# Optimization experiments

Measured on AMD Instinct MI355X. Metric: run time of the kernel, lower is better.

## Reference

```python
import jax, jax.numpy as jnp
import numpy as np

B, H, W, C = 2, 128, 128, 128
NS = 8                      # attn_num_splits
WH, WW = H // NS, W // NS   # window size 16x16
SH, SW = WH // 2, WW // 2   # shift sizes
HID = 2 * C * 4             # ffn hidden (in_channels = 2*d_model, expansion 4)
EPS = 1e-5


def _make_swin_mask():
    # Standard shifted-window attention mask: -100 between different regions.
    img = np.zeros((H, W), np.int32)
    cnt = 0
    for hs in (slice(0, -WH), slice(-WH, -SH), slice(-SH, None)):
        for ws in (slice(0, -WW), slice(-WW, -SW), slice(-SW, None)):
            img[hs, ws] = cnt
            cnt += 1
    ids = img.reshape(NS, WH, NS, WW).transpose(0, 2, 1, 3).reshape(NS * NS, WH * WW)
    mask = np.where(ids[:, None, :] != ids[:, :, None], -100.0, 0.0).astype(np.float32)
    return jnp.asarray(mask)  # (64, 256, 256)


def _layernorm(x, g, b):
    m = jnp.mean(x, axis=-1, keepdims=True)
    v = jnp.mean(jnp.square(x - m), axis=-1, keepdims=True)
    return (x - m) * jax.lax.rsqrt(v + EPS) * g + b


def setup_inputs() -> dict:
    key = jax.random.key(0)
    ks = jax.random.split(key, 8)
    s = 1.0 / np.sqrt(C)
    return {
        "source": jax.random.normal(ks[0], (B, H * W, C), jnp.float32),
        "target": jax.random.normal(ks[1], (B, H * W, C), jnp.float32),
        "Wq": jax.random.normal(ks[2], (C, C), jnp.float32) * s,
        "Wk": jax.random.normal(ks[3], (C, C), jnp.float32) * s,
        "Wv": jax.random.normal(ks[4], (C, C), jnp.float32) * s,
        "Wm": jax.random.normal(ks[5], (C, C), jnp.float32) * s,
        "g1": jnp.ones((C,), jnp.float32),
        "b1": jnp.zeros((C,), jnp.float32),
        "W1": jax.random.normal(ks[6], (2 * C, HID), jnp.float32) * (1.0 / np.sqrt(2 * C)),
        "W2": jax.random.normal(ks[7], (HID, C), jnp.float32) * (1.0 / np.sqrt(HID)),
        "g2": jnp.ones((C,), jnp.float32),
        "b2": jnp.zeros((C,), jnp.float32),
        "shifted_window_attn_mask": _make_swin_mask(),
        "height": H,
        "width": W,
        "attn_num_splits": NS,
    }


def reference(source, target, Wq, Wk, Wv, Wm, g1, b1, W1, W2, g2, b2,
              shifted_window_attn_mask, height, width, attn_num_splits):
    b, L, c = source.shape
    h, w, ns = height, width, attn_num_splits
    wh, ww = h // ns, w // ns
    sh, sw = wh // 2, ww // 2

    q = source @ Wq
    k = target @ Wk
    v = target @ Wv

    def to_windows(x):
        # (b, h*w, c) -> shifted -> (b, nWin, wh*ww, c)
        x = x.reshape(b, h, w, c)
        x = jnp.roll(x, (-sh, -sw), axis=(1, 2))
        x = x.reshape(b, ns, wh, ns, ww, c).transpose(0, 1, 3, 2, 4, 5)
        return x.reshape(b, ns * ns, wh * ww, c)

    qw, kw, vw = to_windows(q), to_windows(k), to_windows(v)
    scores = jnp.einsum('bnlc,bnmc->bnlm', qw, kw) / (c ** 0.5)
    scores = scores + shifted_window_attn_mask[None]  # broadcast over batch
    attn = jax.nn.softmax(scores, axis=-1)
    out = jnp.einsum('bnlm,bnmc->bnlc', attn, vw)

    # merge windows back and undo the shift
    out = out.reshape(b, ns, ns, wh, ww, c).transpose(0, 1, 3, 2, 4, 5).reshape(b, h, w, c)
    out = jnp.roll(out, (sh, sw), axis=(1, 2)).reshape(b, h * w, c)

    message = _layernorm(out @ Wm, g1, b1)
    ffn_in = jnp.concatenate([source, message], axis=-1)
    message = jax.nn.gelu(ffn_in @ W1, approximate=False) @ W2
    message = _layernorm(message, g2, b2)
    return source + message
```

## Files before the change

kernel.cpp:

```cpp
#include <hip/hip_runtime.h>
#include <math.h>
#include <stdint.h>


typedef unsigned short u16;
typedef __attribute__((ext_vector_type(8))) short bf16x8;
typedef __attribute__((ext_vector_type(4))) float f32x4;
typedef __attribute__((ext_vector_type(4))) short u16x4;

__device__ __forceinline__ u16 f2b(float f) {
    unsigned int i = __float_as_uint(f);
    unsigned int r = (i + 0x7fffu + ((i >> 16) & 1u)) >> 16;
    return (u16)r;
}

__device__ __forceinline__ float fast_gelu(float x) {
    float y = fabsf(x) * 0.70710678118f;
    float t = __builtin_amdgcn_rcpf(fmaf(0.3275911f, y, 1.0f));
    float p = fmaf(fmaf(fmaf(fmaf(1.061405429f, t, -1.453152027f), t,
                             1.421413741f), t, -0.284496736f), t, 0.254829592f) * t;
    float e = __expf(-y * y);
    float erf_abs = fmaf(-p, e, 1.0f);
    float s = copysignf(erf_abs, x);
    return 0.5f * x * (1.0f + s);
}

__device__ __forceinline__ void cp16(const void* g, void* l) {
    auto* gp = reinterpret_cast<const __attribute__((address_space(1))) unsigned int*>(
        reinterpret_cast<uintptr_t>(g));
    auto* lp = reinterpret_cast<__attribute__((address_space(3))) unsigned int*>(
        reinterpret_cast<uintptr_t>(l));
    __builtin_amdgcn_global_load_lds(gp, lp, 16, 0, 0);
}

__device__ __forceinline__ int win_map(int gm) {
    int b = gm >> 14, rr = gm & 16383;
    int win = rr >> 8, t = rr & 255;
    int wi = win >> 3, wj = win & 7, i = t >> 4, j = t & 15;
    int h = (wi * 16 + i + 8) & 127;
    int w = (wj * 16 + j + 8) & 127;
    return (b << 14) + h * 128 + w;
}

__global__ __launch_bounds__(256, 2)
void gemm_qkv(const u16* __restrict__ srcb, const u16* __restrict__ tgtb,
              const u16* __restrict__ Bt, u16* __restrict__ qw,
              u16* __restrict__ kw, u16* __restrict__ vwt)
{
    __shared__ __align__(16) u16 SMEM[32768];
    u16* As = SMEM;
    u16* Bs = SMEM + 16384;
    u16* Ts = SMEM;

    const int tid = threadIdx.x;
    const int w = tid >> 6, lane = tid & 63;
    const int lm = lane & 15, q = lane >> 4;
    const int wm = w >> 1, wn = w & 1;
    const int m0 = blockIdx.x * 128;
    const int y = blockIdx.y;
    const u16* Ab = (y == 0) ? srcb : tgtb;

#pragma unroll
    for (int s = 0; s < 4; ++s)
#pragma unroll
        for (int i = 0; i < 2; ++i) {
            int row = w * 32 + i * 16 + (lane >> 2);
            int kc = s * 32 + (lane & 3) * 8;
            cp16(Ab + (size_t)win_map(m0 + row) * 128 + kc,
                 (void*)(As + (s * 128 + w * 32 + i * 16) * 32));
            cp16(Bt + (size_t)(y * 128 + row) * 128 + kc,
                 (void*)(Bs + (s * 128 + w * 32 + i * 16) * 32));
        }
    __syncthreads();

    f32x4 acc[4][4] = {};
#pragma unroll
    for (int s = 0; s < 4; ++s) {
        bf16x8 af[4], bfr[4];
#pragma unroll
        for (int t = 0; t < 4; ++t)
            af[t] = *(const bf16x8*)(As + (s * 128 + wm * 64 + t * 16 + lm) * 32 + q * 8);
#pragma unroll
        for (int t = 0; t < 4; ++t)
            bfr[t] = *(const bf16x8*)(Bs + (s * 128 + wn * 64 + t * 16 + lm) * 32 + q * 8);
#pragma unroll
        for (int mt = 0; mt < 4; ++mt)
#pragma unroll
            for (int nt = 0; nt < 4; ++nt)
                acc[mt][nt] = __builtin_amdgcn_mfma_f32_16x16x32_bf16(
                    af[mt], bfr[nt], acc[mt][nt], 0, 0, 0);
    }

    __syncthreads();
#pragma unroll
    for (int mt = 0; mt < 4; ++mt)
#pragma unroll
        for (int nt = 0; nt < 4; ++nt)
#pragma unroll
            for (int r = 0; r < 4; ++r) {
                int rowl = wm * 64 + mt * 16 + q * 4 + r;
                int col = wn * 64 + nt * 16 + lm;
                int idx = (y == 2) ? col * 136 + rowl : rowl * 136 + col;
                Ts[idx] = f2b(acc[mt][nt][r]);
            }
    __syncthreads();
    const int c8 = (tid & 15) * 8;
#pragma unroll
    for (int i = 0; i < 8; ++i) {
        int rr = i * 16 + (tid >> 4);
        bf16x8 t = *(const bf16x8*)(Ts + rr * 136 + c8);
        if (y == 2) {
            int wix = m0 >> 8, tok0 = m0 & 255;
            *(bf16x8*)(vwt + (size_t)wix * 32768 + (size_t)rr * 256 + tok0 + c8) = t;
        } else {
            u16* Cv = (y == 0) ? qw : kw;
            *(bf16x8*)(Cv + (size_t)(m0 + rr) * 128 + c8) = t;
        }
    }
}

__global__ __launch_bounds__(256, 2)
void gemm_ffn1(const u16* __restrict__ A0, const u16* __restrict__ A1,
               const u16* __restrict__ Bt, u16* __restrict__ C)
{
    __shared__ __align__(16) u16 SMEM[32768];
    u16* As = SMEM;
    u16* Bs = SMEM + 16384;
    u16* Ts = SMEM;

    const int tid = threadIdx.x;
    const int w = tid >> 6, lane = tid & 63;
    const int lm = lane & 15, q = lane >> 4;
    const int wm = w >> 1, wn = w & 1;
    const int m0 = blockIdx.x * 128, n0 = blockIdx.y * 128;

    f32x4 acc[4][4] = {};
#pragma unroll
    for (int kt2 = 0; kt2 < 2; ++kt2) {
        __syncthreads();
        const u16* Ab = kt2 ? A1 : A0;
#pragma unroll
        for (int s = 0; s < 4; ++s)
#pragma unroll
            for (int i = 0; i < 2; ++i) {
                int row = w * 32 + i * 16 + (lane >> 2);
                int kc = s * 32 + (lane & 3) * 8;
                cp16(Ab + (size_t)(m0 + row) * 128 + kc,
                     (void*)(As + (s * 128 + w * 32 + i * 16) * 32));
                cp16(Bt + (size_t)(n0 + row) * 256 + kt2 * 128 + kc,
                     (void*)(Bs + (s * 128 + w * 32 + i * 16) * 32));
            }
        __syncthreads();
#pragma unroll
        for (int s = 0; s < 4; ++s) {
            bf16x8 af[4], bfr[4];
#pragma unroll
            for (int t = 0; t < 4; ++t)
                af[t] = *(const bf16x8*)(As + (s * 128 + wm * 64 + t * 16 + lm) * 32 + q * 8);
#pragma unroll
            for (int t = 0; t < 4; ++t)
                bfr[t] = *(const bf16x8*)(Bs + (s * 128 + wn * 64 + t * 16 + lm) * 32 + q * 8);
#pragma unroll
            for (int mt = 0; mt < 4; ++mt)
#pragma unroll
                for (int nt = 0; nt < 4; ++nt)
                    acc[mt][nt] = __builtin_amdgcn_mfma_f32_16x16x32_bf16(
                        af[mt], bfr[nt], acc[mt][nt], 0, 0, 0);
        }
    }

    __syncthreads();
#pragma unroll
    for (int mt = 0; mt < 4; ++mt)
#pragma unroll
        for (int nt = 0; nt < 4; ++nt)
#pragma unroll
            for (int r = 0; r < 4; ++r) {
                int rowl = wm * 64 + mt * 16 + q * 4 + r;
                int col = wn * 64 + nt * 16 + lm;
                Ts[rowl * 136 + col] = f2b(fast_gelu(acc[mt][nt][r]));
            }
    __syncthreads();
    const int c8 = (tid & 15) * 8;
#pragma unroll
    for (int i = 0; i < 8; ++i) {
        int rr = i * 16 + (tid >> 4);
        bf16x8 t = *(const bf16x8*)(Ts + rr * 136 + c8);
        *(bf16x8*)(C + (size_t)(m0 + rr) * 1024 + n0 + c8) = t;
    }
}

template <int KSTAGES, bool RESID>
__global__ __launch_bounds__(256, 3)
void gemm_ln(const u16* __restrict__ A, const u16* __restrict__ Bt,
             const float* __restrict__ g, const float* __restrict__ bb,
             const float* __restrict__ resid, void* __restrict__ outv)
{
    __shared__ __align__(16) u16 SMEM[25088];
    u16* As = SMEM;
    u16* Bs = SMEM + 8192;
    float* stats = (float*)(SMEM + 24576);
    u16* Ts = SMEM;

    const int tid = threadIdx.x;
    const int w = tid >> 6, lane = tid & 63;
    const int lm = lane & 15, q = lane >> 4;
    const int wm = w >> 1, wn = w & 1;
    const int m0 = blockIdx.x * 64;
    const int K = KSTAGES * 128;

    f32x4 acc[2][4] = {};
#pragma unroll
    for (int kt2 = 0; kt2 < KSTAGES; ++kt2) {
        __syncthreads();
#pragma unroll
        for (int s = 0; s < 4; ++s) {
            int kc = kt2 * 128 + s * 32 + (lane & 3) * 8;
            int arow = w * 16 + (lane >> 2);
            cp16(A + (size_t)(m0 + arow) * K + kc,
                 (void*)(As + (s * 64 + w * 16) * 32));
#pragma unroll
            for (int i = 0; i < 2; ++i) {
                int brow = w * 32 + i * 16 + (lane >> 2);
                cp16(Bt + (size_t)brow * K + kc,
                     (void*)(Bs + (s * 128 + w * 32 + i * 16) * 32));
            }
        }
        __syncthreads();
#pragma unroll
        for (int s = 0; s < 4; ++s) {
            bf16x8 af[2], bfr[4];
#pragma unroll
            for (int t = 0; t < 2; ++t)
                af[t] = *(const bf16x8*)(As + (s * 64 + wm * 32 + t * 16 + lm) * 32 + q * 8);
#pragma unroll
            for (int t = 0; t < 4; ++t)
                bfr[t] = *(const bf16x8*)(Bs + (s * 128 + wn * 64 + t * 16 + lm) * 32 + q * 8);
#pragma unroll
            for (int mt = 0; mt < 2; ++mt)
#pragma unroll
                for (int nt = 0; nt < 4; ++nt)
                    acc[mt][nt] = __builtin_amdgcn_mfma_f32_16x16x32_bf16(
                        af[mt], bfr[nt], acc[mt][nt], 0, 0, 0);
        }
    }

#pragma unroll
    for (int mt = 0; mt < 2; ++mt)
#pragma unroll
        for (int r = 0; r < 4; ++r) {
            float s1 = 0.f, s2 = 0.f;
#pragma unroll
            for (int nt = 0; nt < 4; ++nt) {
                float v = acc[mt][nt][r];
                s1 += v; s2 += v * v;
            }
            s1 += __shfl_xor(s1, 1); s2 += __shfl_xor(s2, 1);
            s1 += __shfl_xor(s1, 2); s2 += __shfl_xor(s2, 2);
            s1 += __shfl_xor(s1, 4); s2 += __shfl_xor(s2, 4);
            s1 += __shfl_xor(s1, 8); s2 += __shfl_xor(s2, 8);
            if (lm == 0) {
                int row = wm * 32 + mt * 16 + q * 4 + r;
                stats[row * 4 + wn * 2] = s1;
                stats[row * 4 + wn * 2 + 1] = s2;
            }
        }
    __syncthreads();

    float gv[4], bv[4];
#pragma unroll
    for (int nt = 0; nt < 4; ++nt) {
        int col = wn * 64 + nt * 16 + lm;
        gv[nt] = g[col]; bv[nt] = bb[col];
    }

#pragma unroll
    for (int mt = 0; mt < 2; ++mt)
#pragma unroll
        for (int r = 0; r < 4; ++r) {
            int row = wm * 32 + mt * 16 + q * 4 + r;
            f32x4 st = *(const f32x4*)(stats + row * 4);
            float mean = (st[0] + st[2]) * (1.f / 128.f);
            float var = fmaxf((st[1] + st[3]) * (1.f / 128.f) - mean * mean, 0.f);
            float rs = rsqrtf(var + 1e-5f);
#pragma unroll
            for (int nt = 0; nt < 4; ++nt) {
                int col = wn * 64 + nt * 16 + lm;
                float yv = (acc[mt][nt][r] - mean) * rs * gv[nt] + bv[nt];
                if (RESID) {
                    size_t gi = (size_t)(m0 + row) * 128 + col;
                    ((float*)outv)[gi] = yv + resid[gi];
                } else {
                    Ts[row * 136 + col] = f2b(yv);
                }
            }
        }
    if (!RESID) {
        __syncthreads();
        const int c8 = (tid & 15) * 8;
#pragma unroll
        for (int i = 0; i < 4; ++i) {
            int rr = i * 16 + (tid >> 4);
            bf16x8 t = *(const bf16x8*)(Ts + rr * 136 + c8);
            *(bf16x8*)((u16*)outv + (size_t)(m0 + rr) * 128 + c8) = t;
        }
    }
}

__global__ __launch_bounds__(256)
void attn_k(const u16* __restrict__ qw, const u16* __restrict__ kw,
            const u16* __restrict__ vt, u16* __restrict__ om)
{
    __shared__ __align__(16) u16 Ps[64 * 264];

    const int tid = threadIdx.x, w = tid >> 6, lane = tid & 63;
    const int lm = lane & 15, q = lane >> 4;
    const int bid = blockIdx.x;
    const int qc = bid & 3, win = (bid >> 2) & 63, b = bid >> 8;
    const int wi = win >> 3, wj = win & 7;
    const int q0 = qc * 64;
    const size_t wbase = (size_t)(b * 64 + win);
    const u16* kwb = kw + wbase * 256 * 128;
    const u16* qwb = qw + wbase * 256 * 128;
    const u16* vtb = vt + wbase * 128 * 256;

    bf16x8 af[4];
    const u16* qrow = qwb + (size_t)(q0 + w * 16 + lm) * 128;
#pragma unroll
    for (int kt = 0; kt < 4; ++kt)
        af[kt] = *(const bf16x8*)(qrow + kt * 32 + q * 8);

    f32x4 s[16];
#pragma unroll
    for (int nt = 0; nt < 16; ++nt) { f32x4 z = {0.f, 0.f, 0.f, 0.f}; s[nt] = z; }
#pragma unroll
    for (int kt = 0; kt < 4; ++kt)
#pragma unroll
        for (int nt = 0; nt < 16; ++nt) {
            bf16x8 bf = *(const bf16x8*)(kwb + (size_t)(nt * 16 + lm) * 128 + kt * 32 + q * 8);
            s[nt] = __builtin_amdgcn_mfma_f32_16x16x32_bf16(af[kt], bf, s[nt], 0, 0, 0);
        }

    int idk[16];
#pragma unroll
    for (int nt = 0; nt < 16; ++nt) {
        int rh = (wi == 7) ? ((nt >= 8) ? 2 : 1) : 0;
        int rw = (wj == 7) ? ((lm >= 8) ? 2 : 1) : 0;
        idk[nt] = rh * 3 + rw;
    }
    const float scale = 0.08838834764831845f;
#pragma unroll
    for (int r = 0; r < 4; ++r) {
        int tq = q0 + w * 16 + q * 4 + r;
        int iq = tq >> 4, jq = tq & 15;
        int rhq = (wi == 7) ? ((iq >= 8) ? 2 : 1) : 0;
        int rwq = (wj == 7) ? ((jq >= 8) ? 2 : 1) : 0;
        int idq = rhq * 3 + rwq;
        float sv[16];
        float mx = -1e30f;
#pragma unroll
        for (int nt = 0; nt < 16; ++nt) {
            float x = s[nt][r] * scale + ((idq != idk[nt]) ? -100.f : 0.f);
            sv[nt] = x; mx = fmaxf(mx, x);
        }
        mx = fmaxf(mx, __shfl_xor(mx, 1));
        mx = fmaxf(mx, __shfl_xor(mx, 2));
        mx = fmaxf(mx, __shfl_xor(mx, 4));
        mx = fmaxf(mx, __shfl_xor(mx, 8));
        float sum = 0.f;
#pragma unroll
        for (int nt = 0; nt < 16; ++nt) { float e = __expf(sv[nt] - mx); sv[nt] = e; sum += e; }
        sum += __shfl_xor(sum, 1);
        sum += __shfl_xor(sum, 2);
        sum += __shfl_xor(sum, 4);
        sum += __shfl_xor(sum, 8);
        float inv = 1.0f / sum;
#pragma unroll
        for (int nt = 0; nt < 16; ++nt)
            Ps[(w * 16 + q * 4 + r) * 264 + nt * 16 + lm] = f2b(sv[nt] * inv);
    }
    __syncthreads();

    f32x4 o[8];
#pragma unroll
    for (int nt = 0; nt < 8; ++nt) { f32x4 z = {0.f, 0.f, 0.f, 0.f}; o[nt] = z; }
#pragma unroll
    for (int tt = 0; tt < 8; ++tt) {
        bf16x8 pf = *(const bf16x8*)(Ps + (w * 16 + lm) * 264 + tt * 32 + q * 8);
#pragma unroll
        for (int nt = 0; nt < 8; ++nt) {
            bf16x8 vf = *(const bf16x8*)(vtb + (size_t)(nt * 16 + lm) * 256 + tt * 32 + q * 8);
            o[nt] = __builtin_amdgcn_mfma_f32_16x16x32_bf16(pf, vf, o[nt], 0, 0, 0);
        }
    }

    __syncthreads();
    u16* Ts = Ps;
#pragma unroll
    for (int r = 0; r < 4; ++r) {
        int rl = w * 16 + q * 4 + r;
#pragma unroll
        for (int nt = 0; nt < 8; ++nt)
            Ts[rl * 136 + nt * 16 + lm] = f2b(o[nt][r]);
    }
    __syncthreads();
    const int c8 = (tid & 15) * 8;
#pragma unroll
    for (int i = 0; i < 4; ++i) {
        int rr = i * 16 + (tid >> 4);
        int t = q0 + rr;
        int ii = t >> 4, jj = t & 15;
        int h = (wi * 16 + ii + 8) & 127;
        int w2 = (wj * 16 + jj + 8) & 127;
        bf16x8 v = *(const bf16x8*)(Ts + rr * 136 + c8);
        *(bf16x8*)(om + ((size_t)b * 16384 + h * 128 + w2) * 128 + c8) = v;
    }
}

__global__ void prep_all(const float* __restrict__ Wq, const float* __restrict__ Wk,
                         const float* __restrict__ Wv, const float* __restrict__ Wm,
                         const float* __restrict__ W1, const float* __restrict__ W2,
                         const float* __restrict__ src, const float* __restrict__ tgt,
                         u16* __restrict__ ws, u16* __restrict__ srcb,
                         u16* __restrict__ tgtb)
{
    int bx = blockIdx.x;
    if (bx < 1792) {
        int idx = bx * 256 + threadIdx.x;
        if (idx < 65536) {
            int m = idx >> 14, e = idx & 16383;
            const float* sp = (m == 0) ? Wq : (m == 1) ? Wk : (m == 2) ? Wv : Wm;
            int k = e >> 7, n = e & 127;
            ws[m * 16384 + n * 128 + k] = f2b(sp[e]);
        } else if (idx < 65536 + 262144) {
            int e = idx - 65536;
            int k = e >> 10, n = e & 1023;
            ws[65536 + n * 256 + k] = f2b(W1[e]);
        } else {
            int e = idx - (65536 + 262144);
            int k = e >> 7, n = e & 127;
            ws[327680 + n * 1024 + k] = f2b(W2[e]);
        }
    } else {
        int idx = (bx - 1792) * 256 + threadIdx.x;
        const float* s; u16* d; int i;
        if (idx < 1048576) { s = src; d = srcb; i = idx * 4; }
        else               { s = tgt; d = tgtb; i = (idx - 1048576) * 4; }
        f32x4 v = *(const f32x4*)(s + i);
        u16x4 o; o[0] = f2b(v[0]); o[1] = f2b(v[1]); o[2] = f2b(v[2]); o[3] = f2b(v[3]);
        *(u16x4*)(d + i) = o;
    }
}

#define OFF_WQT  0u
#define OFF_WMT  49152u
#define OFF_W1T  65536u
#define OFF_W2T  327680u
#define OFF_SRCB 458752u
#define OFF_TGTB 4653056u
#define OFF_QW   8847360u
#define OFF_KW   13041664u
#define OFF_VWT  17235968u
#define OFF_ATTN 21430272u
#define OFF_HID  25624576u
#define OFF_MSGB 8847360u

extern "C" void kernel_launch(void* const* d_in, const int* in_sizes, int n_in,
                              void* d_out, int out_size, void* d_ws, size_t ws_size,
                              hipStream_t stream)
{
    (void)in_sizes; (void)n_in; (void)out_size; (void)ws_size;
    const float* source = (const float*)d_in[0];
    const float* target = (const float*)d_in[1];
    const float* Wq = (const float*)d_in[2];
    const float* Wk = (const float*)d_in[3];
    const float* Wv = (const float*)d_in[4];
    const float* Wm = (const float*)d_in[5];
    const float* g1 = (const float*)d_in[6];
    const float* b1 = (const float*)d_in[7];
    const float* W1 = (const float*)d_in[8];
    const float* W2 = (const float*)d_in[9];
    const float* g2 = (const float*)d_in[10];
    const float* b2 = (const float*)d_in[11];
    u16* ws = (u16*)d_ws;
    float* out = (float*)d_out;

    prep_all<<<9984, 256, 0, stream>>>(Wq, Wk, Wv, Wm, W1, W2, source, target,
                                       ws, ws + OFF_SRCB, ws + OFF_TGTB);
    gemm_qkv<<<dim3(256, 3), 256, 0, stream>>>(
        ws + OFF_SRCB, ws + OFF_TGTB, ws + OFF_WQT,
        ws + OFF_QW, ws + OFF_KW, ws + OFF_VWT);
    attn_k<<<512, 256, 0, stream>>>(ws + OFF_QW, ws + OFF_KW, ws + OFF_VWT, ws + OFF_ATTN);
    gemm_ln<1, false><<<512, 256, 0, stream>>>(
        ws + OFF_ATTN, ws + OFF_WMT, g1, b1, nullptr, (void*)(ws + OFF_MSGB));
    gemm_ffn1<<<dim3(256, 8), 256, 0, stream>>>(
        ws + OFF_SRCB, ws + OFF_MSGB, ws + OFF_W1T, ws + OFF_HID);
    gemm_ln<8, true><<<512, 256, 0, stream>>>(
        ws + OFF_HID, ws + OFF_W2T, g2, b2, source, (void*)out);
}
```

Before: 232.8 us.

## Fuse Wm projection and LayerNorm into attention, switch FFN1 to 32x32 MFMA

The message projection and first LayerNorm move into the attention kernel epilogue, so the separate gemm_ln launch and the round trip of the attention output through global memory go away. FFN1 now uses 32x32x16 MFMA tiles, replaces the erf-based GELU with a cheaper rational approximation, and writes scalar bf16 directly instead of staging through LDS. The prep kernel now iterates in output order, so transposed weight writes become contiguous while the reads become strided. Risks are lower GELU accuracy, uncoalesced 2-byte global stores in the FFN1 and attention epilogues, and the attention kernel reading Wm fragments straight from global memory.

```diff
diff --git a/kernel.cpp b/kernel.cpp
--- a/kernel.cpp
+++ b/kernel.cpp
@@ -6,6 +6,7 @@
 typedef unsigned short u16;
 typedef __attribute__((ext_vector_type(8))) short bf16x8;
 typedef __attribute__((ext_vector_type(4))) float f32x4;
+typedef __attribute__((ext_vector_type(16))) float f32x16;
 typedef __attribute__((ext_vector_type(4))) short u16x4;
 
 __device__ __forceinline__ u16 f2b(float f) {
@@ -14,15 +15,13 @@
     return (u16)r;
 }
 
-__device__ __forceinline__ float fast_gelu(float x) {
+__device__ __forceinline__ float gelu_e(float x) {
     float y = fabsf(x) * 0.70710678118f;
-    float t = __builtin_amdgcn_rcpf(fmaf(0.3275911f, y, 1.0f));
-    float p = fmaf(fmaf(fmaf(fmaf(1.061405429f, t, -1.453152027f), t,
-                             1.421413741f), t, -0.284496736f), t, 0.254829592f) * t;
-    float e = __expf(-y * y);
-    float erf_abs = fmaf(-p, e, 1.0f);
-    float s = copysignf(erf_abs, x);
-    return 0.5f * x * (1.0f + s);
+    float u = fmaf(y, fmaf(y, fmaf(y, fmaf(y, 0.078108f, 0.000972f),
+                                   0.230389f), 0.278393f), 1.0f);
+    u = u * u; u = u * u;
+    float r = __builtin_amdgcn_rcpf(u);
+    return fmaxf(x, 0.f) - 0.5f * fabsf(x) * r;
 }
 
 __device__ __forceinline__ void cp16(const void* g, void* l) {
@@ -126,15 +125,14 @@
     __shared__ __align__(16) u16 SMEM[32768];
     u16* As = SMEM;
     u16* Bs = SMEM + 16384;
-    u16* Ts = SMEM;
 
     const int tid = threadIdx.x;
     const int w = tid >> 6, lane = tid & 63;
-    const int lm = lane & 15, q = lane >> 4;
+    const int l32 = lane & 31, lh = lane >> 5;
     const int wm = w >> 1, wn = w & 1;
     const int m0 = blockIdx.x * 128, n0 = blockIdx.y * 128;
 
-    f32x4 acc[4][4] = {};
+    f32x16 acc[2][2] = {};
 #pragma unroll
     for (int kt2 = 0; kt2 < 2; ++kt2) {
         __syncthreads();
@@ -152,164 +150,46 @@
             }
         __syncthreads();
 #pragma unroll
-        for (int s = 0; s < 4; ++s) {
-            bf16x8 af[4], bfr[4];
-#pragma unroll
-            for (int t = 0; t < 4; ++t)
-                af[t] = *(const bf16x8*)(As + (s * 128 + wm * 64 + t * 16 + lm) * 32 + q * 8);
-#pragma unroll
-            for (int t = 0; t < 4; ++t)
-                bfr[t] = *(const bf16x8*)(Bs + (s * 128 + wn * 64 + t * 16 + lm) * 32 + q * 8);
-#pragma unroll
-            for (int mt = 0; mt < 4; ++mt)
-#pragma unroll
-                for (int nt = 0; nt < 4; ++nt)
-                    acc[mt][nt] = __builtin_amdgcn_mfma_f32_16x16x32_bf16(
-                        af[mt], bfr[nt], acc[mt][nt], 0, 0, 0);
-        }
-    }
-
-    __syncthreads();
-#pragma unroll
-    for (int mt = 0; mt < 4; ++mt)
-#pragma unroll
-        for (int nt = 0; nt < 4; ++nt)
-#pragma unroll
-            for (int r = 0; r < 4; ++r) {
-                int rowl = wm * 64 + mt * 16 + q * 4 + r;
-                int col = wn * 64 + nt * 16 + lm;
-                Ts[rowl * 136 + col] = f2b(fast_gelu(acc[mt][nt][r]));
-            }
-    __syncthreads();
-    const int c8 = (tid & 15) * 8;
-#pragma unroll
-    for (int i = 0; i < 8; ++i) {
-        int rr = i * 16 + (tid >> 4);
-        bf16x8 t = *(const bf16x8*)(Ts + rr * 136 + c8);
-        *(bf16x8*)(C + (size_t)(m0 + rr) * 1024 + n0 + c8) = t;
-    }
-}
-
-template <int KSTAGES, bool RESID>
-__global__ __launch_bounds__(256, 3)
-void gemm_ln(const u16* __restrict__ A, const u16* __restrict__ Bt,
-             const float* __restrict__ g, const float* __restrict__ bb,
-             const float* __restrict__ resid, void* __restrict__ outv)
-{
-    __shared__ __align__(16) u16 SMEM[25088];
-    u16* As = SMEM;
-    u16* Bs = SMEM + 8192;
-    float* stats = (float*)(SMEM + 24576);
-    u16* Ts = SMEM;
-
-    const int tid = threadIdx.x;
-    const int w = tid >> 6, lane = tid & 63;
-    const int lm = lane & 15, q = lane >> 4;
-    const int wm = w >> 1, wn = w & 1;
-    const int m0 = blockIdx.x * 64;
-    const int K = KSTAGES * 128;
-
-    f32x4 acc[2][4] = {};
-#pragma unroll
-    for (int kt2 = 0; kt2 < KSTAGES; ++kt2) {
-        __syncthreads();
-#pragma unroll
-        for (int s = 0; s < 4; ++s) {
-            int kc = kt2 * 128 + s * 32 + (lane & 3) * 8;
-            int arow = w * 16 + (lane >> 2);
-            cp16(A + (size_t)(m0 + arow) * K + kc,
-                 (void*)(As + (s * 64 + w * 16) * 32));
-#pragma unroll
-            for (int i = 0; i < 2; ++i) {
-                int brow = w * 32 + i * 16 + (lane >> 2);
-                cp16(Bt + (size_t)brow * K + kc,
-                     (void*)(Bs + (s * 128 + w * 32 + i * 16) * 32));
-            }
-        }
-        __syncthreads();
-#pragma unroll
-        for (int s = 0; s < 4; ++s) {
-            bf16x8 af[2], bfr[4];
-#pragma unroll
-            for (int t = 0; t < 2; ++t)
-                af[t] = *(const bf16x8*)(As + (s * 64 + wm * 32 + t * 16 + lm) * 32 + q * 8);
-#pragma unroll
-            for (int t = 0; t < 4; ++t)
-                bfr[t] = *(const bf16x8*)(Bs + (s * 128 + wn * 64 + t * 16 + lm) * 32 + q * 8);
-#pragma unroll
-            for (int mt = 0; mt < 2; ++mt)
-#pragma unroll
-                for (int nt = 0; nt < 4; ++nt)
-                    acc[mt][nt] = __builtin_amdgcn_mfma_f32_16x16x32_bf16(
-                        af[mt], bfr[nt], acc[mt][nt], 0, 0, 0);
-        }
+        for (int s = 0; s < 4; ++s)
+#pragma unroll
+            for (int kc = 0; kc < 2; ++kc) {
+                bf16x8 af[2], bfr[2];
+#pragma unroll
+                for (int mt = 0; mt < 2; ++mt)
+                    af[mt] = *(const bf16x8*)(As + (s * 128 + wm * 64 + mt * 32 + l32) * 32
+                                              + kc * 16 + lh * 8);
+#pragma unroll
+                for (int nt = 0; nt < 2; ++nt)
+                    bfr[nt] = *(const bf16x8*)(Bs + (s * 128 + wn * 64 + nt * 32 + l32) * 32
+                                               + kc * 16 + lh * 8);
+#pragma unroll
+                for (int mt = 0; mt < 2; ++mt)
+#pragma unroll
+                    for (int nt = 0; nt < 2; ++nt)
+                        acc[mt][nt] = __builtin_amdgcn_mfma_f32_32x32x16_bf16(
+                            af[mt], bfr[nt], acc[mt][nt], 0, 0, 0);
+            }
     }
 
 #pragma unroll
     for (int mt = 0; mt < 2; ++mt)
 #pragma unroll
-        for (int r = 0; r < 4; ++r) {
-            float s1 = 0.f, s2 = 0.f;
-#pragma unroll
-            for (int nt = 0; nt < 4; ++nt) {
-                float v = acc[mt][nt][r];
-                s1 += v; s2 += v * v;
-            }
-            s1 += __shfl_xor(s1, 1); s2 += __shfl_xor(s2, 1);
-            s1 += __shfl_xor(s1, 2); s2 += __shfl_xor(s2, 2);
-            s1 += __shfl_xor(s1, 4); s2 += __shfl_xor(s2, 4);
-            s1 += __shfl_xor(s1, 8); s2 += __shfl_xor(s2, 8);
-            if (lm == 0) {
-                int row = wm * 32 + mt * 16 + q * 4 + r;
-                stats[row * 4 + wn * 2] = s1;
-                stats[row * 4 + wn * 2 + 1] = s2;
-            }
-        }
-    __syncthreads();
-
-    float gv[4], bv[4];
-#pragma unroll
-    for (int nt = 0; nt < 4; ++nt) {
-        int col = wn * 64 + nt * 16 + lm;
-        gv[nt] = g[col]; bv[nt] = bb[col];
-    }
-
-#pragma unroll
-    for (int mt = 0; mt < 2; ++mt)
-#pragma unroll
-        for (int r = 0; r < 4; ++r) {
-            int row = wm * 32 + mt * 16 + q * 4 + r;
-            f32x4 st = *(const f32x4*)(stats + row * 4);
-            float mean = (st[0] + st[2]) * (1.f / 128.f);
-            float var = fmaxf((st[1] + st[3]) * (1.f / 128.f) - mean * mean, 0.f);
-            float rs = rsqrtf(var + 1e-5f);
-#pragma unroll
-            for (int nt = 0; nt < 4; ++nt) {
-                int col = wn * 64 + nt * 16 + lm;
-                float yv = (acc[mt][nt][r] - mean) * rs * gv[nt] + bv[nt];
-                if (RESID) {
-                    size_t gi = (size_t)(m0 + row) * 128 + col;
-                    ((float*)outv)[gi] = yv + resid[gi];
-                } else {
-                    Ts[row * 136 + col] = f2b(yv);
-                }
-            }
-        }
-    if (!RESID) {
-        __syncthreads();
-        const int c8 = (tid & 15) * 8;
-#pragma unroll
-        for (int i = 0; i < 4; ++i) {
-            int rr = i * 16 + (tid >> 4);
-            bf16x8 t = *(const bf16x8*)(Ts + rr * 136 + c8);
-            *(bf16x8*)((u16*)outv + (size_t)(m0 + rr) * 128 + c8) = t;
-        }
-    }
+        for (int nt = 0; nt < 2; ++nt) {
+            int col = n0 + wn * 64 + nt * 32 + l32;
+            int rbase = m0 + wm * 64 + mt * 32 + 4 * lh;
+#pragma unroll
+            for (int r = 0; r < 16; ++r) {
+                int row = rbase + (r & 3) + 8 * (r >> 2);
+                C[(size_t)row * 1024 + col] = f2b(gelu_e(acc[mt][nt][r]));
+            }
+        }
 }
 
 __global__ __launch_bounds__(256)
-void attn_k(const u16* __restrict__ qw, const u16* __restrict__ kw,
-            const u16* __restrict__ vt, u16* __restrict__ om)
+void attn_msg(const u16* __restrict__ qw, const u16* __restrict__ kw,
+              const u16* __restrict__ vt, const u16* __restrict__ wmt,
+              const float* __restrict__ g, const float* __restrict__ bb,
+              u16* __restrict__ msgb)
 {
     __shared__ __align__(16) u16 Ps[64 * 264];
 
@@ -395,26 +275,158 @@
     }
 
     __syncthreads();
-    u16* Ts = Ps;
+    u16* Ot = Ps;
 #pragma unroll
     for (int r = 0; r < 4; ++r) {
         int rl = w * 16 + q * 4 + r;
 #pragma unroll
         for (int nt = 0; nt < 8; ++nt)
-            Ts[rl * 136 + nt * 16 + lm] = f2b(o[nt][r]);
-    }
-    __syncthreads();
-    const int c8 = (tid & 15) * 8;
-#pragma unroll
-    for (int i = 0; i < 4; ++i) {
-        int rr = i * 16 + (tid >> 4);
-        int t = q0 + rr;
+            Ot[rl * 136 + nt * 16 + lm] = f2b(o[nt][r]);
+    }
+    __syncthreads();
+
+    f32x4 macc[8];
+#pragma unroll
+    for (int n2 = 0; n2 < 8; ++n2) { f32x4 z = {0.f, 0.f, 0.f, 0.f}; macc[n2] = z; }
+#pragma unroll
+    for (int kt = 0; kt < 4; ++kt) {
+        bf16x8 paf = *(const bf16x8*)(Ot + (w * 16 + lm) * 136 + kt * 32 + q * 8);
+#pragma unroll
+        for (int n2 = 0; n2 < 8; ++n2) {
+            bf16x8 wf = *(const bf16x8*)(wmt + (size_t)(n2 * 16 + lm) * 128 + kt * 32 + q * 8);
+            macc[n2] = __builtin_amdgcn_mfma_f32_16x16x32_bf16(paf, wf, macc[n2], 0, 0, 0);
+        }
+    }
+
+    float gv[8], bv[8];
+#pragma unroll
+    for (int n2 = 0; n2 < 8; ++n2) {
+        int col = n2 * 16 + lm;
+        gv[n2] = g[col]; bv[n2] = bb[col];
+    }
+#pragma unroll
+    for (int r = 0; r < 4; ++r) {
+        float s1 = 0.f, s2 = 0.f;
+#pragma unroll
+        for (int n2 = 0; n2 < 8; ++n2) {
+            float v = macc[n2][r];
+            s1 += v; s2 += v * v;
+        }
+        s1 += __shfl_xor(s1, 1); s2 += __shfl_xor(s2, 1);
+        s1 += __shfl_xor(s1, 2); s2 += __shfl_xor(s2, 2);
+        s1 += __shfl_xor(s1, 4); s2 += __shfl_xor(s2, 4);
+        s1 += __shfl_xor(s1, 8); s2 += __shfl_xor(s2, 8);
+        float mean = s1 * (1.f / 128.f);
+        float var = fmaxf(s2 * (1.f / 128.f) - mean * mean, 0.f);
+        float rs = rsqrtf(var + 1e-5f);
+        int t = q0 + w * 16 + q * 4 + r;
         int ii = t >> 4, jj = t & 15;
         int h = (wi * 16 + ii + 8) & 127;
         int w2 = (wj * 16 + jj + 8) & 127;
-        bf16x8 v = *(const bf16x8*)(Ts + rr * 136 + c8);
-        *(bf16x8*)(om + ((size_t)b * 16384 + h * 128 + w2) * 128 + c8) = v;
-    }
+        size_t orow = ((size_t)b * 16384 + h * 128 + w2) * 128;
+#pragma unroll
+        for (int n2 = 0; n2 < 8; ++n2)
+            msgb[orow + n2 * 16 + lm] = f2b((macc[n2][r] - mean) * rs * gv[n2] + bv[n2]);
+    }
+}
+
+__global__ __launch_bounds__(256, 3)
+void gemm_ffn2(const u16* __restrict__ A, const u16* __restrict__ Bt,
+               const float* __restrict__ g, const float* __restrict__ bb,
+               const float* __restrict__ resid, float* __restrict__ outv)
+{
+    __shared__ __align__(16) u16 SMEM[25088];
+    u16* As = SMEM;
+    u16* Bs = SMEM + 8192;
+    float* stats = (float*)(SMEM + 24576);
+
+    const int tid = threadIdx.x;
+    const int w = tid >> 6, lane = tid & 63;
+    const int lm = lane & 15, q = lane >> 4;
+    const int wm = w >> 1, wn = w & 1;
+    const int m0 = blockIdx.x * 64;
+    const int K = 1024;
+
+    f32x4 acc[2][4] = {};
+#pragma unroll
+    for (int kt2 = 0; kt2 < 8; ++kt2) {
+        __syncthreads();
+#pragma unroll
+        for (int s = 0; s < 4; ++s) {
+            int kc = kt2 * 128 + s * 32 + (lane & 3) * 8;
+            int arow = w * 16 + (lane >> 2);
+            cp16(A + (size_t)(m0 + arow) * K + kc,
+                 (void*)(As + (s * 64 + w * 16) * 32));
+#pragma unroll
+            for (int i = 0; i < 2; ++i) {
+                int brow = w * 32 + i * 16 + (lane >> 2);
+                cp16(Bt + (size_t)brow * K + kc,
+                     (void*)(Bs + (s * 128 + w * 32 + i * 16) * 32));
+            }
+        }
+        __syncthreads();
+#pragma unroll
+        for (int s = 0; s < 4; ++s) {
+            bf16x8 af[2], bfr[4];
+#pragma unroll
+            for (int t = 0; t < 2; ++t)
+                af[t] = *(const bf16x8*)(As + (s * 64 + wm * 32 + t * 16 + lm) * 32 + q * 8);
+#pragma unroll
+            for (int t = 0; t < 4; ++t)
+                bfr[t] = *(const bf16x8*)(Bs + (s * 128 + wn * 64 + t * 16 + lm) * 32 + q * 8);
+#pragma unroll
+            for (int mt = 0; mt < 2; ++mt)
+#pragma unroll
+                for (int nt = 0; nt < 4; ++nt)
+                    acc[mt][nt] = __builtin_amdgcn_mfma_f32_16x16x32_bf16(
+                        af[mt], bfr[nt], acc[mt][nt], 0, 0, 0);
+        }
+    }
+
+#pragma unroll
+    for (int mt = 0; mt < 2; ++mt)
+#pragma unroll
+        for (int r = 0; r < 4; ++r) {
+            float s1 = 0.f, s2 = 0.f;
+#pragma unroll
+            for (int nt = 0; nt < 4; ++nt) {
+                float v = acc[mt][nt][r];
+                s1 += v; s2 += v * v;
+            }
+            s1 += __shfl_xor(s1, 1); s2 += __shfl_xor(s2, 1);
+            s1 += __shfl_xor(s1, 2); s2 += __shfl_xor(s2, 2);
+            s1 += __shfl_xor(s1, 4); s2 += __shfl_xor(s2, 4);
+            s1 += __shfl_xor(s1, 8); s2 += __shfl_xor(s2, 8);
+            if (lm == 0) {
+                int row = wm * 32 + mt * 16 + q * 4 + r;
+                stats[row * 4 + wn * 2] = s1;
+                stats[row * 4 + wn * 2 + 1] = s2;
+            }
+        }
+    __syncthreads();
+
+    float gv[4], bv[4];
+#pragma unroll
+    for (int nt = 0; nt < 4; ++nt) {
+        int col = wn * 64 + nt * 16 + lm;
+        gv[nt] = g[col]; bv[nt] = bb[col];
+    }
+#pragma unroll
+    for (int mt = 0; mt < 2; ++mt)
+#pragma unroll
+        for (int r = 0; r < 4; ++r) {
+            int row = wm * 32 + mt * 16 + q * 4 + r;
+            f32x4 st = *(const f32x4*)(stats + row * 4);
+            float mean = (st[0] + st[2]) * (1.f / 128.f);
+            float var = fmaxf((st[1] + st[3]) * (1.f / 128.f) - mean * mean, 0.f);
+            float rs = rsqrtf(var + 1e-5f);
+#pragma unroll
+            for (int nt = 0; nt < 4; ++nt) {
+                int col = wn * 64 + nt * 16 + lm;
+                size_t gi = (size_t)(m0 + row) * 128 + col;
+                outv[gi] = (acc[mt][nt][r] - mean) * rs * gv[nt] + bv[nt] + resid[gi];
+            }
+        }
 }
 
 __global__ void prep_all(const float* __restrict__ Wq, const float* __restrict__ Wk,
@@ -430,16 +442,16 @@
         if (idx < 65536) {
             int m = idx >> 14, e = idx & 16383;
             const float* sp = (m == 0) ? Wq : (m == 1) ? Wk : (m == 2) ? Wv : Wm;
-            int k = e >> 7, n = e & 127;
-            ws[m * 16384 + n * 128 + k] = f2b(sp[e]);
-        } else if (idx < 65536 + 262144) {
+            int n = e >> 7, k = e & 127;
+            ws[m * 16384 + n * 128 + k] = f2b(sp[k * 128 + n]);
+        } else if (idx < 327680) {
             int e = idx - 65536;
-            int k = e >> 10, n = e & 1023;
-            ws[65536 + n * 256 + k] = f2b(W1[e]);
+            int n = e >> 8, k = e & 255;
+            ws[65536 + n * 256 + k] = f2b(W1[k * 1024 + n]);
         } else {
-            int e = idx - (65536 + 262144);
-            int k = e >> 7, n = e & 127;
-            ws[327680 + n * 1024 + k] = f2b(W2[e]);
+            int e = idx - 327680;
+            int n = e >> 10, k = e & 1023;
+            ws[327680 + n * 1024 + k] = f2b(W2[k * 128 + n]);
         }
     } else {
         int idx = (bx - 1792) * 256 + threadIdx.x;
@@ -461,9 +473,8 @@
 #define OFF_QW   8847360u
 #define OFF_KW   13041664u
 #define OFF_VWT  17235968u
-#define OFF_ATTN 21430272u
+#define OFF_MSGB 21430272u
 #define OFF_HID  25624576u
-#define OFF_MSGB 8847360u
 
 extern "C" void kernel_launch(void* const* d_in, const int* in_sizes, int n_in,
                               void* d_out, int out_size, void* d_ws, size_t ws_size,
@@ -490,11 +501,11 @@
     gemm_qkv<<<dim3(256, 3), 256, 0, stream>>>(
         ws + OFF_SRCB, ws + OFF_TGTB, ws + OFF_WQT,
         ws + OFF_QW, ws + OFF_KW, ws + OFF_VWT);
-    attn_k<<<512, 256, 0, stream>>>(ws + OFF_QW, ws + OFF_KW, ws + OFF_VWT, ws + OFF_ATTN);
-    gemm_ln<1, false><<<512, 256, 0, stream>>>(
-        ws + OFF_ATTN, ws + OFF_WMT, g1, b1, nullptr, (void*)(ws + OFF_MSGB));
+    attn_msg<<<512, 256, 0, stream>>>(
+        ws + OFF_QW, ws + OFF_KW, ws + OFF_VWT, ws + OFF_WMT, g1, b1,
+        ws + OFF_MSGB);
     gemm_ffn1<<<dim3(256, 8), 256, 0, stream>>>(
         ws + OFF_SRCB, ws + OFF_MSGB, ws + OFF_W1T, ws + OFF_HID);
-    gemm_ln<8, true><<<512, 256, 0, stream>>>(
-        ws + OFF_HID, ws + OFF_W2T, g2, b2, source, (void*)out);
-}
+    gemm_ffn2<<<512, 256, 0, stream>>>(
+        ws + OFF_HID, ws + OFF_W2T, g2, b2, source, out);
+}
```

Result: no change. 232.5 us (-0.2%).
